# Performance work log

Hardware: AMD Instinct MI355X
Metric: run time of the kernel (lower is better)

Reference implementation:

```python
import jax, jax.numpy as jnp
import numpy as np

ATTEN_DIM = 64

def setup_inputs() -> dict:
    key = jax.random.key(0)
    ks = jax.random.split(key, 7)
    b, c, h, w = 16, 2048, 32, 32
    d_att, d_emb = 64, 64
    x = jax.random.normal(ks[0], (b, c, h, w), dtype=jnp.float32)
    # 1x1 conv == per-position linear; store weights as [out, in]
    scale = 1.0 / np.sqrt(c)
    wq = jax.random.normal(ks[1], (d_att, c), dtype=jnp.float32) * scale
    wk = jax.random.normal(ks[2], (d_att, c), dtype=jnp.float32) * scale
    wv = jax.random.normal(ks[3], (d_emb, c), dtype=jnp.float32) * scale
    bq = jnp.zeros((d_att,), dtype=jnp.float32)
    bk = jnp.zeros((d_att,), dtype=jnp.float32)
    bv = jnp.zeros((d_emb,), dtype=jnp.float32)
    return {"x": x, "wq": wq, "bq": bq, "wk": wk, "bk": bk, "wv": wv, "bv": bv}


def reference(x, wq, bq, wk, bk, wv, bv):
    b, c, h, w = x.shape
    # 1x1 conv projections: [b,c,h,w] x [d,c] -> [b,d,h,w]
    q = jnp.einsum('bchw,dc->bdhw', x, wq) + bq[None, :, None, None]
    k = jnp.einsum('bchw,dc->bdhw', x, wk) + bk[None, :, None, None]
    v = jnp.einsum('bchw,dc->bdhw', x, wv) + bv[None, :, None, None]
    # full non-local attention scores [b, h, w, h, w]
    atten = jnp.einsum('bcxy,bcij->bxyij', q, k) / ATTEN_DIM  # NOTE: module divides by atten_dim, not sqrt
    atten = jax.nn.softmax(atten.reshape(b, h, w, h * w), axis=-1).reshape(b, h, w, h, w)
    out = jnp.einsum('bxyij,bdij->bxyd', atten, v)
    return jnp.transpose(out, (0, 3, 1, 2))  # [b, emb_dim, h, w]
```

## Files before the change

### kernel.cpp

```cpp
#include <hip/hip_runtime.h>

typedef float f32x4 __attribute__((ext_vector_type(4)));
typedef short s16x8 __attribute__((ext_vector_type(8)));
typedef unsigned u32x4 __attribute__((ext_vector_type(4)));
typedef unsigned short u16;
typedef unsigned short u16x8 __attribute__((ext_vector_type(8)));

__device__ __forceinline__ u16 f2bf(float f) {
  unsigned u = __builtin_bit_cast(unsigned, f);
  u += 0x7fffu + ((u >> 16) & 1u);
  return (u16)(u >> 16);
}

__device__ __forceinline__ unsigned cvt_pk_bf16(float a, float b) {
  unsigned r;
  asm("v_cvt_pk_bf16_f32 %0, %1, %2" : "=v"(r) : "v"(a), "v"(b));
  return r;
}

#define AS1 __attribute__((address_space(1)))
#define AS3 __attribute__((address_space(3)))
#define GLD16(g, l) __builtin_amdgcn_global_load_lds((const AS1 unsigned int*)(g), (AS3 unsigned int*)(l), 16, 0, 0)

#define CEXP 0.0225421101f

__global__ __launch_bounds__(256) void prepack_w(
    const float* __restrict__ wq, const float* __restrict__ wk, const float* __restrict__ wv,
    u16* __restrict__ Wpk)
{
  const int d = blockIdx.x;
  const int t = threadIdx.x;
  const int kc = t >> 3, blk = t & 7;
  const int key = (d >> 1) & 7;
  const float* src = (d < 64) ? (wq + (size_t)d * 2048)
                   : (d < 128) ? (wk + (size_t)(d - 64) * 2048)
                               : (wv + (size_t)(d - 128) * 2048);
  const float* s8 = src + kc * 64 + ((blk ^ key) << 3);
  u16x8 o;
#pragma unroll
  for (int j = 0; j < 8; ++j) o[j] = f2bf(s8[j]);
  *(u16x8*)(Wpk + ((size_t)(kc * 192 + d) << 6) + (blk << 3)) = o;
}

__global__ __launch_bounds__(512) void qkv_proj(
    const float* __restrict__ x, const u16* __restrict__ Wpk,
    const float* __restrict__ bq, const float* __restrict__ bk, const float* __restrict__ bv,
    u16* __restrict__ Qo, u16* __restrict__ Ko, u16* __restrict__ Vt)
{
  const int b   = blockIdx.x >> 4;
  const int p0  = (blockIdx.x & 15) * 64;
  const int tid = threadIdx.x;
  const int lane = tid & 63;
  const int wid  = tid >> 6;
  const int l15 = lane & 15, l4 = lane >> 4;
  const int wm = wid & 1, wn = wid >> 1;

  __shared__ __align__(16) u16 lA[4][64 * 64];
  __shared__ __align__(16) u16 lB[4][192 * 64];

  const int pg = lane & 15;
  const int kb = wid * 4 + (lane >> 4);
  const int k0 = kb * 4;
  const int ww = wid - 4;

  f32x4 acc[2][3];
#pragma unroll
  for (int m = 0; m < 2; ++m)
#pragma unroll
    for (int n = 0; n < 3; ++n) acc[m][n] = (f32x4)(0.0f);

  const float* xb = x + (size_t)b * 2048 * 1024 + p0 + pg * 4;
  float4 SA[8], SB[8];

  auto xload2 = [&](int c, float4 (&S)[8]) {
#pragma unroll
    for (int cc = 0; cc < 2; ++cc) {
      const float* g = xb + (size_t)((c + cc) * 64 + k0) * 1024;
#pragma unroll
      for (int r = 0; r < 4; ++r) S[cc * 4 + r] = *(const float4*)(g + r * 1024);
    }
  };
  auto xstore2 = [&](int c, float4 (&S)[8]) {
#pragma unroll
    for (int cc = 0; cc < 2; ++cc) {
      const int slot = (c + cc) & 3;
#pragma unroll
      for (int col = 0; col < 4; ++col) {
        int p = pg * 4 + col;
        unsigned lo = cvt_pk_bf16(S[cc * 4 + 0][col], S[cc * 4 + 1][col]);
        unsigned hi = cvt_pk_bf16(S[cc * 4 + 2][col], S[cc * 4 + 3][col]);
        int swz = ((kb >> 1) ^ ((p >> 1) & 7)) & 7;
        char* dst = (char*)&lA[0][0] + slot * 8192 + p * 128 + (swz << 4) + (kb & 1) * 8;
        *(uint2*)dst = make_uint2(lo, hi);
      }
    }
  };
  auto wissue2 = [&](int c) {
#pragma unroll
    for (int cc = 0; cc < 2; ++cc) {
      const int slot = (c + cc) & 3;
      const u16* g = Wpk + (size_t)(c + cc) * 12288 + lane * 8;
#pragma unroll
      for (int j = 0; j < 6; ++j) {
        int q = ww * 6 + j;
        GLD16(g + q * 512, &lB[0][0] + slot * 12288 + q * 512);
      }
    }
  };
  auto domfma = [&](int slot) {
#pragma unroll
    for (int ks = 0; ks < 2; ++ks) {
      s16x8 af[2], bfv[3];
#pragma unroll
      for (int m = 0; m < 2; ++m) {
        int p = wm * 32 + m * 16 + l15;
        int swz = ((ks * 4 + l4) ^ ((p >> 1) & 7)) & 7;
        af[m] = *(const s16x8*)((const char*)&lA[0][0] + slot * 8192 + p * 128 + (swz << 4));
      }
#pragma unroll
      for (int n = 0; n < 3; ++n) {
        int d = wn * 48 + n * 16 + l15;
        int swz = ((ks * 4 + l4) ^ ((d >> 1) & 7)) & 7;
        bfv[n] = *(const s16x8*)((const char*)&lB[0][0] + slot * 24576 + d * 128 + (swz << 4));
      }
#pragma unroll
      for (int m = 0; m < 2; ++m)
#pragma unroll
        for (int n = 0; n < 3; ++n)
          acc[m][n] = __builtin_amdgcn_mfma_f32_16x16x32_bf16(af[m], bfv[n], acc[m][n], 0, 0, 0);
    }
  };
  auto barrier = [&]() {
    if (wid < 4) asm volatile("s_waitcnt lgkmcnt(0)" ::: "memory");
    else         asm volatile("s_waitcnt vmcnt(0) lgkmcnt(0)" ::: "memory");
    __builtin_amdgcn_sched_barrier(0);
    __builtin_amdgcn_s_barrier();
    __builtin_amdgcn_sched_barrier(0);
  };
  auto step = [&](int t, float4 (&Sl)[8], float4 (&Ss)[8]) {
    if (wid < 4) { if (t < 14) xload2(2 * t + 4, Sl); }
    else         { if (t < 15) wissue2(2 * t + 2); }
    __builtin_amdgcn_s_setprio(1);
    domfma((2 * t) & 3);
    domfma((2 * t + 1) & 3);
    __builtin_amdgcn_s_setprio(0);
    if (wid < 4 && t < 15) xstore2(2 * t + 2, Ss);
    barrier();
  };

  if (wid < 4) { xload2(0, SA); xload2(2, SB); xstore2(0, SA); }
  else         { wissue2(0); }
  barrier();

  for (int tt = 0; tt < 8; ++tt) {
    step(2 * tt,     SA, SB);
    step(2 * tt + 1, SB, SA);
  }

#pragma unroll
  for (int n = 0; n < 3; ++n) {
    const int dg = wn * 48 + n * 16 + l15;
    const int wi = dg >> 6, dl = dg & 63;
    const float* bsrc = (wi == 0) ? bq : (wi == 1) ? bk : bv;
    const float bias = bsrc[dl];
#pragma unroll
    for (int m = 0; m < 2; ++m) {
      const int pl = wm * 32 + m * 16 + l4 * 4;
      f32x4 a = acc[m][n];
      if (wi == 0) {
        u16* dst = Qo + ((size_t)b * 1024 + p0 + pl) * 64 + dl;
#pragma unroll
        for (int r = 0; r < 4; ++r) dst[(size_t)r * 64] = f2bf((a[r] + bias) * CEXP);
      } else if (wi == 1) {
#pragma unroll
        for (int r = 0; r < 4; ++r) {
          const int p = p0 + pl + r;
          const int p2 = (p & ~28) | ((p & 8) >> 1) | ((p & 16) >> 1) | ((p & 4) << 2);
          Ko[((size_t)b * 1024 + p2) * 64 + (((dl >> 3) ^ ((p2 >> 1) & 7)) << 3) + (dl & 7)]
            = f2bf(a[r] + bias);
        }
      } else {
        const int pk0 = p0 + pl;
        ushort4 hh;
        hh.x = f2bf(a[0] + bias); hh.y = f2bf(a[1] + bias);
        hh.z = f2bf(a[2] + bias); hh.w = f2bf(a[3] + bias);
        u16* dst = Vt + ((size_t)b * 64 + dl) * 1024 + (pk0 & ~127)
                 + (((((pk0 >> 3) & 15) ^ ((dl & 7) << 1)) & 15) << 3) + (pk0 & 7);
        *(ushort4*)dst = hh;
      }
    }
  }
}

__global__ __launch_bounds__(256) void attn_kernel(
    const u16* __restrict__ Qg, const u16* __restrict__ Kg,
    const u16* __restrict__ Vg, float* __restrict__ Po, float* __restrict__ lp)
{
  const int bid = blockIdx.x;
  const int b  = bid >> 5;
  const int qt = (bid >> 1) & 15;
  const int h  = bid & 1;
  const int q0 = qt * 64;
  const int tid = threadIdx.x;
  const int lane = tid & 63;
  const int w = tid >> 6;
  const int l15 = lane & 15, l4 = lane >> 4;
  const int qb = q0 + w * 16;

  __shared__ __align__(16) u16 lK[2][128 * 64];
  __shared__ __align__(16) u16 lV[2][64 * 128];

  s16x8 qa[2];
#pragma unroll
  for (int ks = 0; ks < 2; ++ks)
    qa[ks] = *(const s16x8*)(Qg + ((size_t)b * 1024 + qb + l15) * 64 + ks * 32 + l4 * 8);

  const u16* Kb = Kg + (size_t)b * 65536;
  const u16* Vb = Vg + (size_t)b * 65536;

  float l_run = 0.f;
  f32x4 oacc[4];
#pragma unroll
  for (int n = 0; n < 4; ++n) oacc[n] = (f32x4)(0.0f);

  auto kv_issue = [&](int tile, int buf) {
    const int pk0 = tile * 128;
#pragma unroll
    for (int jj = 0; jj < 4; ++jj)
      GLD16(Kb + (size_t)(pk0 + w * 32 + jj * 8) * 64 + lane * 8,
            (char*)&lK[buf][0] + (w * 4 + jj) * 1024);
#pragma unroll
    for (int jj = 0; jj < 4; ++jj)
      GLD16(Vb + (size_t)(w * 16 + jj * 4 + (lane >> 4)) * 1024 + pk0 + (lane & 15) * 8,
            (char*)&lV[buf][0] + (w * 4 + jj) * 1024);
  };

  auto compute = [&](int buf) {
    f32x4 sacc[8];
#pragma unroll
    for (int n = 0; n < 8; ++n) sacc[n] = (f32x4)(0.0f);
    __builtin_amdgcn_s_setprio(1);
#pragma unroll
    for (int ks = 0; ks < 2; ++ks) {
#pragma unroll
      for (int n = 0; n < 8; ++n) {
        int row = n * 16 + l15;
        s16x8 kv = *(const s16x8*)(&lK[buf][0] + row * 64 +
                     (((ks * 4 + l4) ^ ((row >> 1) & 7)) << 3));
        sacc[n] = __builtin_amdgcn_mfma_f32_16x16x32_bf16(kv, qa[ks], sacc[n], 0, 0, 0);
      }
    }
    __builtin_amdgcn_s_setprio(0);

    unsigned c[8][2];
    float psum = 0.f;
#pragma unroll
    for (int n = 0; n < 8; ++n) {
      float e0 = exp2f(sacc[n][0]);
      float e1 = exp2f(sacc[n][1]);
      float e2 = exp2f(sacc[n][2]);
      float e3 = exp2f(sacc[n][3]);
      psum += (e0 + e1) + (e2 + e3);
      c[n][0] = cvt_pk_bf16(e0, e1);
      c[n][1] = cvt_pk_bf16(e2, e3);
    }
    psum += __shfl_xor(psum, 16);
    psum += __shfl_xor(psum, 32);
    l_run += psum;

    __builtin_amdgcn_s_setprio(1);
#pragma unroll
    for (int ks = 0; ks < 4; ++ks) {
      u32x4 t;
      t[0] = c[2 * ks][0];
      t[1] = c[2 * ks][1];
      t[2] = c[2 * ks + 1][0];
      t[3] = c[2 * ks + 1][1];
      s16x8 pfr = __builtin_bit_cast(s16x8, t);
#pragma unroll
      for (int n = 0; n < 4; ++n) {
        int row = n * 16 + l15;
        s16x8 vv = *(const s16x8*)(&lV[buf][0] + row * 128 +
                     (((ks * 4 + l4) ^ ((row & 7) << 1)) << 3));
        oacc[n] = __builtin_amdgcn_mfma_f32_16x16x32_bf16(pfr, vv, oacc[n], 0, 0, 0);
      }
    }
    __builtin_amdgcn_s_setprio(0);
  };

  const int t0 = h * 4;
  kv_issue(t0, 0);
  kv_issue(t0 + 1, 1);
  asm volatile("s_waitcnt vmcnt(8)" ::: "memory");
  __builtin_amdgcn_sched_barrier(0);
  __builtin_amdgcn_s_barrier();
  __builtin_amdgcn_sched_barrier(0);

  for (int ic = 0; ic < 4; ++ic) {
    compute(ic & 1);
    if (ic < 3) {
      __builtin_amdgcn_sched_barrier(0);
      __builtin_amdgcn_s_barrier();
      __builtin_amdgcn_sched_barrier(0);
      if (ic + 2 < 4) {
        kv_issue(t0 + ic + 2, ic & 1);
        asm volatile("s_waitcnt vmcnt(8)" ::: "memory");
      } else {
        asm volatile("s_waitcnt vmcnt(0)" ::: "memory");
      }
      __builtin_amdgcn_sched_barrier(0);
      __builtin_amdgcn_s_barrier();
      __builtin_amdgcn_sched_barrier(0);
    }
  }

  float lr[4];
#pragma unroll
  for (int r = 0; r < 4; ++r) lr[r] = __shfl(l_run, l4 * 4 + r);

#pragma unroll
  for (int n = 0; n < 4; ++n) {
    const int d = n * 16 + l15;
    float4 o;
    o.x = oacc[n][0]; o.y = oacc[n][1]; o.z = oacc[n][2]; o.w = oacc[n][3];
    *(float4*)(Po + (((size_t)h * 16 + b) * 64 + d) * 1024 + q0 + w * 16 + l4 * 4) = o;
  }
  if (l15 == 0) {
#pragma unroll
    for (int r = 0; r < 4; ++r)
      lp[((size_t)h * 16 + b) * 1024 + qb + l4 * 4 + r] = lr[r];
  }
}

__global__ __launch_bounds__(256) void attn_merge(
    const float* __restrict__ Po, const float* __restrict__ lp, float* __restrict__ out)
{
  const int i = (blockIdx.x * 256 + threadIdx.x) * 4;
  float4 a = *(const float4*)(Po + i);
  float4 c = *(const float4*)(Po + 1048576 + i);
  const int b = i >> 16;
  const int p = i & 1023;
  const float* l0 = lp + b * 1024 + p;
  const float* l1 = lp + 16384 + b * 1024 + p;
  float4 o;
  o.x = (a.x + c.x) / (l0[0] + l1[0]);
  o.y = (a.y + c.y) / (l0[1] + l1[1]);
  o.z = (a.z + c.z) / (l0[2] + l1[2]);
  o.w = (a.w + c.w) / (l0[3] + l1[3]);
  *(float4*)(out + i) = o;
}

extern "C" void kernel_launch(void* const* d_in, const int* in_sizes, int n_in,
                              void* d_out, int out_size, void* d_ws, size_t ws_size,
                              hipStream_t stream) {
  const float* x  = (const float*)d_in[0];
  const float* wq = (const float*)d_in[1];
  const float* bq = (const float*)d_in[2];
  const float* wk = (const float*)d_in[3];
  const float* bk = (const float*)d_in[4];
  const float* wv = (const float*)d_in[5];
  const float* bv = (const float*)d_in[6];
  float* out = (float*)d_out;

  u16* Qo  = (u16*)d_ws;
  u16* Ko  = Qo + (size_t)16 * 1024 * 64;
  u16* Vt  = Ko + (size_t)16 * 1024 * 64;
  u16* Wpk = Vt + (size_t)16 * 1024 * 64;
  float* Po = (float*)(Wpk + (size_t)32 * 192 * 64);
  float* lpart = Po + (size_t)2 * 16 * 64 * 1024;

  prepack_w<<<192, 256, 0, stream>>>(wq, wk, wv, Wpk);
  qkv_proj<<<256, 512, 0, stream>>>(x, Wpk, bq, bk, bv, Qo, Ko, Vt);
  attn_kernel<<<512, 256, 0, stream>>>(Qo, Ko, Vt, Po, lpart);
  attn_merge<<<1024, 256, 0, stream>>>(Po, lpart, out);
}
```

Baseline: 55.40 us.

## Fuse split-KV merge into attention kernel via shared-memory reduction

The attention kernel now runs both KV halves inside one 512-thread block, two groups of four waves, instead of two separate blocks. The partial outputs and row sums are combined through shared memory at the end, so the separate merge kernel, its launch and the global round-trip of the partial results are removed. In exchange the grid shrinks to 256 blocks that each use 128KB of LDS, which lowers occupancy and parallelism across CUs.

```diff
diff --git a/kernel.cpp b/kernel.cpp
--- a/kernel.cpp
+++ b/kernel.cpp
@@ -192,28 +192,29 @@
   }
 }
 
-__global__ __launch_bounds__(256) void attn_kernel(
+__global__ __launch_bounds__(512) void attn_kernel(
     const u16* __restrict__ Qg, const u16* __restrict__ Kg,
-    const u16* __restrict__ Vg, float* __restrict__ Po, float* __restrict__ lp)
+    const u16* __restrict__ Vg, float* __restrict__ out)
 {
   const int bid = blockIdx.x;
-  const int b  = bid >> 5;
-  const int qt = (bid >> 1) & 15;
-  const int h  = bid & 1;
+  const int b  = bid >> 4;
+  const int qt = bid & 15;
   const int q0 = qt * 64;
   const int tid = threadIdx.x;
   const int lane = tid & 63;
-  const int w = tid >> 6;
+  const int wid = tid >> 6;
+  const int h = wid >> 2;
+  const int w = wid & 3;
   const int l15 = lane & 15, l4 = lane >> 4;
-  const int qb = q0 + w * 16;
-
-  __shared__ __align__(16) u16 lK[2][128 * 64];
-  __shared__ __align__(16) u16 lV[2][64 * 128];
+
+  __shared__ __align__(16) char smem[131072];
+  char* const gbase = smem + h * 65536;
 
   s16x8 qa[2];
 #pragma unroll
   for (int ks = 0; ks < 2; ++ks)
-    qa[ks] = *(const s16x8*)(Qg + ((size_t)b * 1024 + qb + l15) * 64 + ks * 32 + l4 * 8);
+    qa[ks] = *(const s16x8*)(Qg + ((size_t)b * 1024 + q0 + w * 16 + l15) * 64
+                             + ks * 32 + l4 * 8);
 
   const u16* Kb = Kg + (size_t)b * 65536;
   const u16* Vb = Vg + (size_t)b * 65536;
@@ -228,14 +229,16 @@
 #pragma unroll
     for (int jj = 0; jj < 4; ++jj)
       GLD16(Kb + (size_t)(pk0 + w * 32 + jj * 8) * 64 + lane * 8,
-            (char*)&lK[buf][0] + (w * 4 + jj) * 1024);
+            gbase + buf * 16384 + (w * 4 + jj) * 1024);
 #pragma unroll
     for (int jj = 0; jj < 4; ++jj)
       GLD16(Vb + (size_t)(w * 16 + jj * 4 + (lane >> 4)) * 1024 + pk0 + (lane & 15) * 8,
-            (char*)&lV[buf][0] + (w * 4 + jj) * 1024);
+            gbase + 32768 + buf * 16384 + (w * 4 + jj) * 1024);
   };
 
   auto compute = [&](int buf) {
+    const u16* kB = (const u16*)(gbase + buf * 16384);
+    const u16* vB = (const u16*)(gbase + 32768 + buf * 16384);
     f32x4 sacc[8];
 #pragma unroll
     for (int n = 0; n < 8; ++n) sacc[n] = (f32x4)(0.0f);
@@ -245,7 +248,7 @@
 #pragma unroll
       for (int n = 0; n < 8; ++n) {
         int row = n * 16 + l15;
-        s16x8 kv = *(const s16x8*)(&lK[buf][0] + row * 64 +
+        s16x8 kv = *(const s16x8*)(kB + row * 64 +
                      (((ks * 4 + l4) ^ ((row >> 1) & 7)) << 3));
         sacc[n] = __builtin_amdgcn_mfma_f32_16x16x32_bf16(kv, qa[ks], sacc[n], 0, 0, 0);
       }
@@ -280,7 +283,7 @@
 #pragma unroll
       for (int n = 0; n < 4; ++n) {
         int row = n * 16 + l15;
-        s16x8 vv = *(const s16x8*)(&lV[buf][0] + row * 128 +
+        s16x8 vv = *(const s16x8*)(vB + row * 128 +
                      (((ks * 4 + l4) ^ ((row & 7) << 1)) << 3));
         oacc[n] = __builtin_amdgcn_mfma_f32_16x16x32_bf16(pfr, vv, oacc[n], 0, 0, 0);
       }
@@ -318,36 +321,31 @@
 #pragma unroll
   for (int r = 0; r < 4; ++r) lr[r] = __shfl(l_run, l4 * 4 + r);
 
-#pragma unroll
-  for (int n = 0; n < 4; ++n) {
-    const int d = n * 16 + l15;
-    float4 o;
-    o.x = oacc[n][0]; o.y = oacc[n][1]; o.z = oacc[n][2]; o.w = oacc[n][3];
-    *(float4*)(Po + (((size_t)h * 16 + b) * 64 + d) * 1024 + q0 + w * 16 + l4 * 4) = o;
-  }
-  if (l15 == 0) {
-#pragma unroll
-    for (int r = 0; r < 4; ++r)
-      lp[((size_t)h * 16 + b) * 1024 + qb + l4 * 4 + r] = lr[r];
-  }
-}
-
-__global__ __launch_bounds__(256) void attn_merge(
-    const float* __restrict__ Po, const float* __restrict__ lp, float* __restrict__ out)
-{
-  const int i = (blockIdx.x * 256 + threadIdx.x) * 4;
-  float4 a = *(const float4*)(Po + i);
-  float4 c = *(const float4*)(Po + 1048576 + i);
-  const int b = i >> 16;
-  const int p = i & 1023;
-  const float* l0 = lp + b * 1024 + p;
-  const float* l1 = lp + 16384 + b * 1024 + p;
-  float4 o;
-  o.x = (a.x + c.x) / (l0[0] + l1[0]);
-  o.y = (a.y + c.y) / (l0[1] + l1[1]);
-  o.z = (a.z + c.z) / (l0[2] + l1[2]);
-  o.w = (a.w + c.w) / (l0[3] + l1[3]);
-  *(float4*)(out + i) = o;
+  __syncthreads();
+  if (h == 1) {
+    float* mrg = (float*)smem + (tid - 256) * 20;
+#pragma unroll
+    for (int n = 0; n < 4; ++n) *(f32x4*)(mrg + n * 4) = oacc[n];
+#pragma unroll
+    for (int r = 0; r < 4; ++r) mrg[16 + r] = lr[r];
+  }
+  __syncthreads();
+  if (h == 0) {
+    const float* mrg = (const float*)smem + tid * 20;
+    float lt[4];
+#pragma unroll
+    for (int r = 0; r < 4; ++r) lt[r] = lr[r] + mrg[16 + r];
+#pragma unroll
+    for (int n = 0; n < 4; ++n) {
+      f32x4 o1 = *(const f32x4*)(mrg + n * 4);
+      float4 o;
+      o.x = (oacc[n][0] + o1[0]) / lt[0];
+      o.y = (oacc[n][1] + o1[1]) / lt[1];
+      o.z = (oacc[n][2] + o1[2]) / lt[2];
+      o.w = (oacc[n][3] + o1[3]) / lt[3];
+      *(float4*)(out + ((size_t)b * 64 + n * 16 + l15) * 1024 + q0 + w * 16 + l4 * 4) = o;
+    }
+  }
 }
 
 extern "C" void kernel_launch(void* const* d_in, const int* in_sizes, int n_in,
@@ -366,11 +364,8 @@
   u16* Ko  = Qo + (size_t)16 * 1024 * 64;
   u16* Vt  = Ko + (size_t)16 * 1024 * 64;
   u16* Wpk = Vt + (size_t)16 * 1024 * 64;
-  float* Po = (float*)(Wpk + (size_t)32 * 192 * 64);
-  float* lpart = Po + (size_t)2 * 16 * 64 * 1024;
 
   prepack_w<<<192, 256, 0, stream>>>(wq, wk, wv, Wpk);
   qkv_proj<<<256, 512, 0, stream>>>(x, Wpk, bq, bk, bv, Qo, Ko, Vt);
-  attn_kernel<<<512, 256, 0, stream>>>(Qo, Ko, Vt, Po, lpart);
-  attn_merge<<<1024, 256, 0, stream>>>(Po, lpart, out);
-}
+  attn_kernel<<<256, 512, 0, stream>>>(Qo, Ko, Vt, out);
+}
```

Measured after the change: 53.20 us, median of 2. -4.0%, faster.
